# Kernel tuning notes

Measured on AMD Instinct MI355X. Metric: run time of the kernel, lower is better.

## Reference

```python
import jax, jax.numpy as jnp
import numpy as np

NEG_SLOPE = 0.01  # F.leaky_relu default


def _unfold3(x):
    # x: [B,C,H,W] -> [B,C,9,H,W] of 3x3 neighborhoods (zero pad 1)
    B, C, H, W = x.shape
    xp = jnp.pad(x, ((0, 0), (0, 0), (1, 1), (1, 1)))
    return jnp.stack([xp[:, :, i:i + H, j:j + W] for i in range(3) for j in range(3)], axis=2)


def _resize_bilinear(img, oh, ow):
    # torch F.interpolate mode='bilinear', align_corners=False, antialias=False
    B, C, H, W = img.shape
    if oh == H and ow == W:
        return img
    def coords(out, inn):
        c = jnp.maximum((jnp.arange(out, dtype=jnp.float32) + 0.5) * (inn / out) - 0.5, 0.0)
        i0 = jnp.floor(c).astype(jnp.int32)
        i1 = jnp.minimum(i0 + 1, inn - 1)
        w = c - i0.astype(jnp.float32)
        return i0, i1, w
    i0, i1, wh = coords(oh, H)
    row = img[:, :, i0, :] * (1.0 - wh)[None, None, :, None] + img[:, :, i1, :] * wh[None, None, :, None]
    j0, j1, ww = coords(ow, W)
    return row[:, :, :, j0] * (1.0 - ww) + row[:, :, :, j1] * ww


def _up2_nearest(x):
    # F.interpolate scale_factor=2 (default mode='nearest')
    return jnp.repeat(jnp.repeat(x, 2, axis=2), 2, axis=3)


def _leaky(x):
    return jnp.where(x >= 0, x, NEG_SLOPE * x)


def _pac_conv(x, guide, w):
    # PacConv2d (gaussian kernel, k=3, stride=1, pad=1, bias=False)
    g_unf = _unfold3(guide)                      # [B,Cg,9,H,W]
    diff = g_unf - guide[:, :, None]             # f_j - f_i
    kern = jnp.exp(-0.5 * jnp.sum(diff * diff, axis=1))  # [B,9,H,W]
    x_unf = _unfold3(x)                          # [B,Ci,9,H,W]
    wk = w.reshape(w.shape[0], w.shape[1], 9)    # [Co,Ci,9]
    return jnp.einsum('oik,bikhw,bkhw->bohw', wk, x_unf, kern)


def setup_inputs() -> dict:
    key = jax.random.key(0)
    ks = jax.random.split(key, 8)
    B, Cx, Hx, Wx = 4, 384, 32, 32
    Hg = Wg = 512
    x = jax.random.normal(ks[0], (B, Cx, Hx, Wx), dtype=jnp.float32)
    guide = jax.random.uniform(ks[1], (B, 3, Hg, Wg), dtype=jnp.float32)
    lin_w = jax.random.normal(ks[2], (16, 384, 1, 1), dtype=jnp.float32) * 0.05
    lin_b = jax.random.normal(ks[3], (16,), dtype=jnp.float32) * 0.05
    chans = [16, 4, 4, 4, 1]
    w0 = jax.random.normal(ks[4], (chans[1], chans[0], 3, 3), dtype=jnp.float32) * 0.1
    w1 = jax.random.normal(ks[5], (chans[2], chans[1], 3, 3), dtype=jnp.float32) * 0.1
    w2 = jax.random.normal(ks[6], (chans[3], chans[2], 3, 3), dtype=jnp.float32) * 0.1
    w3 = jax.random.normal(ks[7], (chans[4], chans[3], 3, 3), dtype=jnp.float32) * 0.1
    return {"x": x, "guide": guide, "lin_w": lin_w, "lin_b": lin_b,
            "w0": w0, "w1": w1, "w2": w2, "w3": w3}


def reference(x, guide, lin_w, lin_b, w0, w1, w2, w3):
    # crop guide to multiple of 16 (module uses shape[-1] for both dims)
    s = (guide.shape[-1] // 16) * 16
    guide = guide[..., :s, :s]
    # 1x1 conv + leaky relu
    x = jnp.einsum('oi,bihw->bohw', lin_w[:, :, 0, 0], x) + lin_b[None, :, None, None]
    x = _leaky(x)
    ws = [w0, w1, w2, w3]
    n = len(ws)
    Hg, Wg = guide.shape[2], guide.shape[3]
    for i in range(n):
        f = 2 ** (n - 1 - i)
        g = _resize_bilinear(guide, Hg // f, Wg // f)
        x = _up2_nearest(x)
        x = _pac_conv(x, g, ws[i])
        if i < n - 1:
            x = _leaky(x)
    return jax.nn.sigmoid(x)
```

## Files before the change

### kernel.cpp

```cpp
#include <hip/hip_runtime.h>
#include <math.h>

#define NEG_SLOPE 0.01f

__device__ inline float bilin(const float* __restrict__ gp, float scale, int r, int c) {
    float ch = fmaxf((r + 0.5f) * scale - 0.5f, 0.f);
    float cw = fmaxf((c + 0.5f) * scale - 0.5f, 0.f);
    int h0 = (int)ch, w0 = (int)cw;
    int h1 = min(h0 + 1, 511), w1 = min(w0 + 1, 511);
    float fh = ch - (float)h0, fw = cw - (float)w0;
    float v00 = gp[h0 * 512 + w0], v01 = gp[h0 * 512 + w1];
    float v10 = gp[h1 * 512 + w0], v11 = gp[h1 * 512 + w1];
    float top = v00 + (v01 - v00) * fw;
    float bot = v10 + (v11 - v10) * fw;
    return top + (bot - top) * fh;
}

__global__ void __launch_bounds__(256)
prep_kernel(const float* __restrict__ x, const float* __restrict__ lw,
            const float* __restrict__ lb, float* __restrict__ x16,
            const float* __restrict__ g, float* __restrict__ g64p,
            float* __restrict__ g128p, float* __restrict__ g256p) {
    int bid = blockIdx.x;
    if (bid < 256) {
        int idx = bid * 256 + threadIdx.x;
        int hw = idx & 1023, co = (idx >> 10) & 15, bb = idx >> 14;
        const float* xp = x + bb * 384 * 1024 + hw;
        const float* wp = lw + co * 384;
        float a0 = 0.f, a1 = 0.f, a2 = 0.f, a3 = 0.f;
        for (int ci = 0; ci < 384; ci += 4) {
            a0 = fmaf(wp[ci],     xp[(ci)     * 1024], a0);
            a1 = fmaf(wp[ci + 1], xp[(ci + 1) * 1024], a1);
            a2 = fmaf(wp[ci + 2], xp[(ci + 2) * 1024], a2);
            a3 = fmaf(wp[ci + 3], xp[(ci + 3) * 1024], a3);
        }
        float acc = lb[co] + ((a0 + a1) + (a2 + a3));
        x16[idx] = acc >= 0.f ? acc : NEG_SLOPE * acc;
    } else {
        int idx = (bid - 256) * 256 + threadIdx.x;
        int R; float scale; float* outp; int o;
        if (idx < 786432)      { R = 256; scale = 2.f; outp = g256p; o = idx; }
        else if (idx < 983040) { R = 128; scale = 4.f; outp = g128p; o = idx - 786432; }
        else                   { R = 64;  scale = 8.f; outp = g64p;  o = idx - 983040; }
        int c = o % R;
        int r = (o / R) % R;
        int bc = o / (R * R);
        outp[o] = bilin(g + (size_t)bc * 262144, scale, r, c);
    }
}

template <int Ci, int Co>
__device__ inline void pac_lds(const float* __restrict__ sx, int BXr, int BXc, int NX,
                               const float* __restrict__ sg, int BGr, int BGc, int NG,
                               const float* __restrict__ sw, float* __restrict__ so,
                               int BOr, int BOc, int NO, int RES) {
    const int NG2 = NG * NG, NX2 = NX * NX, NO2 = NO * NO;
    for (int i = threadIdx.x; i < NO2; i += 256) {
        int r = i / NO, c = i % NO;
        int gh = BOr + r, gw = BOc + c;
        float acc[Co];
#pragma unroll
        for (int co = 0; co < Co; ++co) acc[co] = 0.f;
        if (gh >= 0 && gh < RES && gw >= 0 && gw < RES) {
            int lc0 = (gh - BGr) * NG + (gw - BGc);
            float gc0 = sg[lc0], gc1 = sg[NG2 + lc0], gc2 = sg[2 * NG2 + lc0];
#pragma unroll
            for (int tt = 0; tt < 9; ++tt) {
                int hh = gh + tt / 3 - 1, ww = gw + tt % 3 - 1;
                if (hh < 0 || hh >= RES || ww < 0 || ww >= RES) continue;
                int lt = (hh - BGr) * NG + (ww - BGc);
                float d0 = sg[lt] - gc0;
                float d1 = sg[NG2 + lt] - gc1;
                float d2 = sg[2 * NG2 + lt] - gc2;
                float k = __expf(-0.5f * (d0 * d0 + d1 * d1 + d2 * d2));
                int lx = ((hh >> 1) - BXr) * NX + ((ww >> 1) - BXc);
#pragma unroll
                for (int ci = 0; ci < Ci; ++ci) {
                    float xv = sx[ci * NX2 + lx] * k;
#pragma unroll
                    for (int co = 0; co < Co; ++co)
                        acc[co] = fmaf(sw[(co * Ci + ci) * 9 + tt], xv, acc[co]);
                }
            }
        }
#pragma unroll
        for (int co = 0; co < Co; ++co) {
            float v = acc[co];
            so[co * NO2 + i] = v >= 0.f ? v : NEG_SLOPE * v;
        }
    }
}

__global__ void __launch_bounds__(256)
pac_mid_kernel(const float* __restrict__ x16g, const float* __restrict__ g64p,
               const float* __restrict__ g128p,
               const float* __restrict__ w0, const float* __restrict__ w1,
               float* __restrict__ x1g) {
    __shared__ float smem[3100];
    float* sw0   = smem;
    float* sw1   = smem + 576;
    float* sx16  = smem + 720;
    float* sg64  = smem + 1296;
    float* sg128 = smem + 1728;
    float* sx0   = smem + 2700;

    int bid = blockIdx.x;
    int b = bid >> 6;
    int t = (bid >> 3) & 7;
    int u = bid & 7;

    const int BXr = 4 * t - 1,  BXc = 4 * u - 1;
    const int BG0r = 8 * t - 2, BG0c = 8 * u - 2;
    const int B0r = 8 * t - 1,  B0c = 8 * u - 1;
    const int BG1r = 16 * t - 1, BG1c = 16 * u - 1;

    for (int i = threadIdx.x; i < 576; i += 256) sw0[i] = w0[i];
    for (int i = threadIdx.x; i < 144; i += 256) sw1[i] = w1[i];
    for (int i = threadIdx.x; i < 576; i += 256) {
        int ci = i / 36, rem = i % 36, r = rem / 6, c = rem % 6;
        int gr = BXr + r, gc = BXc + c;
        float v = 0.f;
        if (gr >= 0 && gr < 32 && gc >= 0 && gc < 32)
            v = x16g[((b * 16 + ci) << 10) + (gr << 5) + gc];
        sx16[i] = v;
    }
    for (int i = threadIdx.x; i < 432; i += 256) {
        int ch = i / 144, rem = i % 144, r = rem / 12, c = rem % 12;
        int gr = BG0r + r, gc = BG0c + c;
        float v = 0.f;
        if (gr >= 0 && gr < 64 && gc >= 0 && gc < 64)
            v = g64p[(b * 3 + ch) * 4096 + (gr << 6) + gc];
        sg64[i] = v;
    }
    for (int i = threadIdx.x; i < 972; i += 256) {
        int ch = i / 324, rem = i % 324, r = rem / 18, c = rem % 18;
        int gr = BG1r + r, gc = BG1c + c;
        float v = 0.f;
        if (gr >= 0 && gr < 128 && gc >= 0 && gc < 128)
            v = g128p[(b * 3 + ch) * 16384 + (gr << 7) + gc];
        sg128[i] = v;
    }
    __syncthreads();

    pac_lds<16, 4>(sx16, BXr, BXc, 6, sg64, BG0r, BG0c, 12, sw0, sx0, B0r, B0c, 10, 64);
    __syncthreads();

    {
        int i = threadIdx.x;
        int r = i >> 4, c = i & 15;
        int gh = 16 * t + r, gw = 16 * u + c;
        int lc0 = (gh - BG1r) * 18 + (gw - BG1c);
        float gc0 = sg128[lc0], gc1 = sg128[324 + lc0], gc2 = sg128[648 + lc0];
        float acc[4] = {0.f, 0.f, 0.f, 0.f};
#pragma unroll
        for (int tt = 0; tt < 9; ++tt) {
            int hh = gh + tt / 3 - 1, ww = gw + tt % 3 - 1;
            if (hh < 0 || hh >= 128 || ww < 0 || ww >= 128) continue;
            int lt = (hh - BG1r) * 18 + (ww - BG1c);
            float d0 = sg128[lt] - gc0;
            float d1 = sg128[324 + lt] - gc1;
            float d2 = sg128[648 + lt] - gc2;
            float k = __expf(-0.5f * (d0 * d0 + d1 * d1 + d2 * d2));
            int lx = ((hh >> 1) - B0r) * 10 + ((ww >> 1) - B0c);
#pragma unroll
            for (int ci = 0; ci < 4; ++ci) {
                float xv = sx0[ci * 100 + lx] * k;
#pragma unroll
                for (int co = 0; co < 4; ++co)
                    acc[co] = fmaf(sw1[(co * 4 + ci) * 9 + tt], xv, acc[co]);
            }
        }
#pragma unroll
        for (int co = 0; co < 4; ++co) {
            float v = acc[co];
            v = v >= 0.f ? v : NEG_SLOPE * v;
            x1g[((b * 4 + co) << 14) + (gh << 7) + gw] = v;
        }
    }
}

template <int Ci, int Co, int R, int ACT>
__global__ void __launch_bounds__(256)
pac_stage(const float* __restrict__ x, const float* __restrict__ g,
          const float* __restrict__ wk, float* __restrict__ out) {
    __shared__ float sw[Co * Ci * 9];
    for (int i = threadIdx.x; i < Co * Ci * 9; i += 256) sw[i] = wk[i];
    __syncthreads();

    constexpr int HW = R * R;
    constexpr int Rh = R / 2;
    constexpr int HWh = Rh * Rh;
    int idx = blockIdx.x * 256 + threadIdx.x;
    int w = idx & (R - 1);
    int h = (idx / R) & (R - 1);
    int b = idx / HW;

    const float* gb = g + (size_t)b * 3 * HW;
    int ctr = h * R + w;
    float gc0 = gb[ctr];
    float gc1 = gb[HW + ctr];
    float gc2 = gb[2 * HW + ctr];

    float acc[Co];
#pragma unroll
    for (int co = 0; co < Co; ++co) acc[co] = 0.f;

    const float* xb = x + (size_t)b * Ci * HWh;

#pragma unroll
    for (int t = 0; t < 9; ++t) {
        int dh = t / 3 - 1, dw = t % 3 - 1;
        int hh = h + dh, ww = w + dw;
        if (hh < 0 || hh >= R || ww < 0 || ww >= R) continue;
        int tap = hh * R + ww;
        float d0 = gb[tap] - gc0;
        float d1 = gb[HW + tap] - gc1;
        float d2 = gb[2 * HW + tap] - gc2;
        float k = __expf(-0.5f * (d0 * d0 + d1 * d1 + d2 * d2));
        const float* xp = xb + (hh >> 1) * Rh + (ww >> 1);
#pragma unroll
        for (int ci = 0; ci < Ci; ++ci) {
            float xv = xp[ci * HWh] * k;
#pragma unroll
            for (int co = 0; co < Co; ++co)
                acc[co] = fmaf(sw[(co * Ci + ci) * 9 + t], xv, acc[co]);
        }
    }

#pragma unroll
    for (int co = 0; co < Co; ++co) {
        float v = acc[co];
        if (ACT == 0) v = v >= 0.f ? v : NEG_SLOPE * v;
        else          v = 1.0f / (1.0f + __expf(-v));
        out[(size_t)(b * Co + co) * HW + ctr] = v;
    }
}

__global__ void __launch_bounds__(256)
pac512_quad_kernel(const float* __restrict__ x2g, const float* __restrict__ guide,
                   const float* __restrict__ w3, float* __restrict__ out) {
    __shared__ float sw[36];
    if (threadIdx.x < 36) sw[threadIdx.x] = w3[threadIdx.x];
    __syncthreads();

    int idx = blockIdx.x * 256 + threadIdx.x;
    int qw = idx & 255;
    int qh = (idx >> 8) & 255;
    int b = idx >> 16;
    int h0 = qh << 1, w0 = qw << 1;

    const float* gb = guide + (size_t)b * 3 * 262144;
    const float* xb = x2g + (size_t)b * 4 * 65536;

    float gw[3][4][4];
#pragma unroll
    for (int rr = 0; rr < 4; ++rr) {
        int gr = h0 - 1 + rr;
        bool rok = (gr >= 0 && gr < 512);
#pragma unroll
        for (int cc = 0; cc < 4; ++cc) {
            int gc = w0 - 1 + cc;
            bool ok = rok && (gc >= 0 && gc < 512);
            int a = (gr << 9) + gc;
#pragma unroll
            for (int ch = 0; ch < 3; ++ch)
                gw[ch][rr][cc] = ok ? gb[ch * 262144 + a] : 0.f;
        }
    }
    float xw[4][3][3];
#pragma unroll
    for (int rr = 0; rr < 3; ++rr) {
        int xr = qh - 1 + rr;
        bool rok = (xr >= 0 && xr < 256);
#pragma unroll
        for (int cc = 0; cc < 3; ++cc) {
            int xc = qw - 1 + cc;
            bool ok = rok && (xc >= 0 && xc < 256);
            int a = (xr << 8) + xc;
#pragma unroll
            for (int ci = 0; ci < 4; ++ci)
                xw[ci][rr][cc] = ok ? xb[ci * 65536 + a] : 0.f;
        }
    }

    float* ob = out + (size_t)b * 262144;
#pragma unroll
    for (int dr = 0; dr < 2; ++dr) {
#pragma unroll
        for (int dc = 0; dc < 2; ++dc) {
            float gc0 = gw[0][dr + 1][dc + 1];
            float gc1 = gw[1][dr + 1][dc + 1];
            float gc2 = gw[2][dr + 1][dc + 1];
            float acc = 0.f;
#pragma unroll
            for (int tt = 0; tt < 9; ++tt) {
                const int th = tt / 3, tc = tt % 3;
                int hh = h0 + dr + th - 1, ww = w0 + dc + tc - 1;
                if (hh < 0 || hh >= 512 || ww < 0 || ww >= 512) continue;
                float d0 = gw[0][dr + th][dc + tc] - gc0;
                float d1 = gw[1][dr + th][dc + tc] - gc1;
                float d2 = gw[2][dr + th][dc + tc] - gc2;
                float k = __expf(-0.5f * (d0 * d0 + d1 * d1 + d2 * d2));
                const int xr = ((dr + th - 1) >> 1) + 1;
                const int xc = ((dc + tc - 1) >> 1) + 1;
#pragma unroll
                for (int ci = 0; ci < 4; ++ci)
                    acc = fmaf(sw[ci * 9 + tt], xw[ci][xr][xc] * k, acc);
            }
            ob[((h0 + dr) << 9) + (w0 + dc)] = 1.0f / (1.0f + __expf(-acc));
        }
    }
}

extern "C" void kernel_launch(void* const* d_in, const int* in_sizes, int n_in,
                              void* d_out, int out_size, void* d_ws, size_t ws_size,
                              hipStream_t stream) {
    const float* x     = (const float*)d_in[0];
    const float* guide = (const float*)d_in[1];
    const float* lin_w = (const float*)d_in[2];
    const float* lin_b = (const float*)d_in[3];
    const float* w0    = (const float*)d_in[4];
    const float* w1    = (const float*)d_in[5];
    const float* w2    = (const float*)d_in[6];
    const float* w3    = (const float*)d_in[7];
    float* out = (float*)d_out;

    float* ws    = (float*)d_ws;
    float* x16   = ws;
    float* g64p  = x16 + 65536;
    float* g128p = g64p + 49152;
    float* g256p = g128p + 196608;
    float* x1    = g256p + 786432;
    float* x2    = x1 + 262144;

    prep_kernel<<<4288, 256, 0, stream>>>(x, lin_w, lin_b, x16, guide, g64p, g128p, g256p);
    pac_mid_kernel<<<256, 256, 0, stream>>>(x16, g64p, g128p, w0, w1, x1);
    pac_stage<4, 4, 256, 0><<<1024, 256, 0, stream>>>(x1, g256p, w2, x2);
    pac512_quad_kernel<<<1024, 256, 0, stream>>>(x2, guide, w3, out);
}
```

Measured before the change: 120.0 us.

## Fuse last two PAC stages into one LDS-tiled kernel and simplify bilinear downsampling

Replaces the separate 256-resolution PAC stage and the 512-resolution quad kernel with one kernel per 16x16 output tile. It stages the guide, the downsampled guide and the x1 halo in LDS, computes the x2 tile with overlap, then the final output, so the x2 intermediate never goes through global memory and one launch is removed. It also replaces the general bilinear resize with exact 2-tap averages, since downscaling by an integer factor with align_corners=False lands on midpoints, and makes the pac_lds tile sizes compile-time template parameters. The cost is redundant halo recomputation of x2 and more LDS use per block.

```diff
diff --git a/kernel.cpp b/kernel.cpp
--- a/kernel.cpp
+++ b/kernel.cpp
@@ -2,19 +2,6 @@
 #include <math.h>
 
 #define NEG_SLOPE 0.01f
-
-__device__ inline float bilin(const float* __restrict__ gp, float scale, int r, int c) {
-    float ch = fmaxf((r + 0.5f) * scale - 0.5f, 0.f);
-    float cw = fmaxf((c + 0.5f) * scale - 0.5f, 0.f);
-    int h0 = (int)ch, w0 = (int)cw;
-    int h1 = min(h0 + 1, 511), w1 = min(w0 + 1, 511);
-    float fh = ch - (float)h0, fw = cw - (float)w0;
-    float v00 = gp[h0 * 512 + w0], v01 = gp[h0 * 512 + w1];
-    float v10 = gp[h1 * 512 + w0], v11 = gp[h1 * 512 + w1];
-    float top = v00 + (v01 - v00) * fw;
-    float bot = v10 + (v11 - v10) * fw;
-    return top + (bot - top) * fh;
-}
 
 __global__ void __launch_bounds__(256)
 prep_kernel(const float* __restrict__ x, const float* __restrict__ lw,
@@ -38,23 +25,37 @@
         x16[idx] = acc >= 0.f ? acc : NEG_SLOPE * acc;
     } else {
         int idx = (bid - 256) * 256 + threadIdx.x;
-        int R; float scale; float* outp; int o;
-        if (idx < 786432)      { R = 256; scale = 2.f; outp = g256p; o = idx; }
-        else if (idx < 983040) { R = 128; scale = 4.f; outp = g128p; o = idx - 786432; }
-        else                   { R = 64;  scale = 8.f; outp = g64p;  o = idx - 983040; }
-        int c = o % R;
-        int r = (o / R) % R;
-        int bc = o / (R * R);
-        outp[o] = bilin(g + (size_t)bc * 262144, scale, r, c);
-    }
-}
-
-template <int Ci, int Co>
-__device__ inline void pac_lds(const float* __restrict__ sx, int BXr, int BXc, int NX,
-                               const float* __restrict__ sg, int BGr, int BGc, int NG,
+        if (idx < 786432) {
+            int o = idx;
+            int c = o & 255, r = (o >> 8) & 255, bc = o >> 16;
+            const float2* gp2 = (const float2*)(g + (size_t)bc * 262144);
+            float2 a = gp2[(2 * r) * 256 + c];
+            float2 b = gp2[(2 * r + 1) * 256 + c];
+            g256p[o] = 0.25f * ((a.x + a.y) + (b.x + b.y));
+        } else if (idx < 983040) {
+            int o = idx - 786432;
+            int c = o & 127, r = (o >> 7) & 127, bc = o >> 14;
+            const float* gp = g + (size_t)bc * 262144;
+            int a0 = (4 * r + 1) * 512 + 4 * c + 1;
+            int a1 = a0 + 512;
+            g128p[o] = 0.25f * ((gp[a0] + gp[a0 + 1]) + (gp[a1] + gp[a1 + 1]));
+        } else {
+            int o = idx - 983040;
+            int c = o & 63, r = (o >> 6) & 63, bc = o >> 12;
+            const float* gp = g + (size_t)bc * 262144;
+            int a0 = (8 * r + 3) * 512 + 8 * c + 3;
+            int a1 = a0 + 512;
+            g64p[o] = 0.25f * ((gp[a0] + gp[a0 + 1]) + (gp[a1] + gp[a1 + 1]));
+        }
+    }
+}
+
+template <int Ci, int Co, int NX, int NG, int NO, int RES>
+__device__ inline void pac_lds(const float* __restrict__ sx, int BXr, int BXc,
+                               const float* __restrict__ sg, int BGr, int BGc,
                                const float* __restrict__ sw, float* __restrict__ so,
-                               int BOr, int BOc, int NO, int RES) {
-    const int NG2 = NG * NG, NX2 = NX * NX, NO2 = NO * NO;
+                               int BOr, int BOc) {
+    constexpr int NG2 = NG * NG, NX2 = NX * NX, NO2 = NO * NO;
     for (int i = threadIdx.x; i < NO2; i += 256) {
         int r = i / NO, c = i % NO;
         int gh = BOr + r, gw = BOc + c;
@@ -142,7 +143,7 @@
     }
     __syncthreads();
 
-    pac_lds<16, 4>(sx16, BXr, BXc, 6, sg64, BG0r, BG0c, 12, sw0, sx0, B0r, B0c, 10, 64);
+    pac_lds<16, 4, 6, 12, 10, 64>(sx16, BXr, BXc, sg64, BG0r, BG0c, sw0, sx0, B0r, B0c);
     __syncthreads();
 
     {
@@ -179,136 +180,84 @@
     }
 }
 
-template <int Ci, int Co, int R, int ACT>
 __global__ void __launch_bounds__(256)
-pac_stage(const float* __restrict__ x, const float* __restrict__ g,
-          const float* __restrict__ wk, float* __restrict__ out) {
-    __shared__ float sw[Co * Ci * 9];
-    for (int i = threadIdx.x; i < Co * Ci * 9; i += 256) sw[i] = wk[i];
-    __syncthreads();
-
-    constexpr int HW = R * R;
-    constexpr int Rh = R / 2;
-    constexpr int HWh = Rh * Rh;
-    int idx = blockIdx.x * 256 + threadIdx.x;
-    int w = idx & (R - 1);
-    int h = (idx / R) & (R - 1);
-    int b = idx / HW;
-
-    const float* gb = g + (size_t)b * 3 * HW;
-    int ctr = h * R + w;
-    float gc0 = gb[ctr];
-    float gc1 = gb[HW + ctr];
-    float gc2 = gb[2 * HW + ctr];
-
-    float acc[Co];
-#pragma unroll
-    for (int co = 0; co < Co; ++co) acc[co] = 0.f;
-
-    const float* xb = x + (size_t)b * Ci * HWh;
-
-#pragma unroll
-    for (int t = 0; t < 9; ++t) {
-        int dh = t / 3 - 1, dw = t % 3 - 1;
-        int hh = h + dh, ww = w + dw;
-        if (hh < 0 || hh >= R || ww < 0 || ww >= R) continue;
-        int tap = hh * R + ww;
-        float d0 = gb[tap] - gc0;
-        float d1 = gb[HW + tap] - gc1;
-        float d2 = gb[2 * HW + tap] - gc2;
-        float k = __expf(-0.5f * (d0 * d0 + d1 * d1 + d2 * d2));
-        const float* xp = xb + (hh >> 1) * Rh + (ww >> 1);
-#pragma unroll
-        for (int ci = 0; ci < Ci; ++ci) {
-            float xv = xp[ci * HWh] * k;
-#pragma unroll
-            for (int co = 0; co < Co; ++co)
-                acc[co] = fmaf(sw[(co * Ci + ci) * 9 + t], xv, acc[co]);
-        }
-    }
-
-#pragma unroll
-    for (int co = 0; co < Co; ++co) {
-        float v = acc[co];
-        if (ACT == 0) v = v >= 0.f ? v : NEG_SLOPE * v;
-        else          v = 1.0f / (1.0f + __expf(-v));
-        out[(size_t)(b * Co + co) * HW + ctr] = v;
-    }
-}
-
-__global__ void __launch_bounds__(256)
-pac512_quad_kernel(const float* __restrict__ x2g, const float* __restrict__ guide,
-                   const float* __restrict__ w3, float* __restrict__ out) {
-    __shared__ float sw[36];
-    if (threadIdx.x < 36) sw[threadIdx.x] = w3[threadIdx.x];
-    __syncthreads();
-
-    int idx = blockIdx.x * 256 + threadIdx.x;
-    int qw = idx & 255;
-    int qh = (idx >> 8) & 255;
-    int b = idx >> 16;
-    int h0 = qh << 1, w0 = qw << 1;
+pac_de_kernel(const float* __restrict__ x1g, const float* __restrict__ guide,
+              const float* __restrict__ g256p,
+              const float* __restrict__ w2, const float* __restrict__ w3,
+              float* __restrict__ out) {
+    __shared__ float smem[2128];
+    float* sw2   = smem;
+    float* sw3   = smem + 144;
+    float* sg512 = smem + 180;
+    float* sg256 = smem + 1152;
+    float* sx1   = smem + 1584;
+    float* sx2   = smem + 1728;
+
+    int bid = blockIdx.x;
+    int b = bid >> 10;
+    int t = (bid >> 5) & 31;
+    int u = bid & 31;
+
+    const int B1r = 4 * t - 1,   B1c = 4 * u - 1;
+    const int BG2r = 8 * t - 2,  BG2c = 8 * u - 2;
+    const int B2r = 8 * t - 1,   B2c = 8 * u - 1;
+    const int BG3r = 16 * t - 1, BG3c = 16 * u - 1;
 
     const float* gb = guide + (size_t)b * 3 * 262144;
-    const float* xb = x2g + (size_t)b * 4 * 65536;
-
-    float gw[3][4][4];
-#pragma unroll
-    for (int rr = 0; rr < 4; ++rr) {
-        int gr = h0 - 1 + rr;
-        bool rok = (gr >= 0 && gr < 512);
-#pragma unroll
-        for (int cc = 0; cc < 4; ++cc) {
-            int gc = w0 - 1 + cc;
-            bool ok = rok && (gc >= 0 && gc < 512);
-            int a = (gr << 9) + gc;
-#pragma unroll
-            for (int ch = 0; ch < 3; ++ch)
-                gw[ch][rr][cc] = ok ? gb[ch * 262144 + a] : 0.f;
-        }
-    }
-    float xw[4][3][3];
-#pragma unroll
-    for (int rr = 0; rr < 3; ++rr) {
-        int xr = qh - 1 + rr;
-        bool rok = (xr >= 0 && xr < 256);
-#pragma unroll
-        for (int cc = 0; cc < 3; ++cc) {
-            int xc = qw - 1 + cc;
-            bool ok = rok && (xc >= 0 && xc < 256);
-            int a = (xr << 8) + xc;
+
+    for (int i = threadIdx.x; i < 972; i += 256) {
+        int ch = i / 324, rem = i % 324, r = rem / 18, c = rem % 18;
+        int gr = BG3r + r, gc = BG3c + c;
+        float v = 0.f;
+        if (gr >= 0 && gr < 512 && gc >= 0 && gc < 512)
+            v = gb[ch * 262144 + (gr << 9) + gc];
+        sg512[i] = v;
+    }
+    for (int i = threadIdx.x; i < 432; i += 256) {
+        int ch = i / 144, rem = i % 144, r = rem / 12, c = rem % 12;
+        int gr = BG2r + r, gc = BG2c + c;
+        float v = 0.f;
+        if (gr >= 0 && gr < 256 && gc >= 0 && gc < 256)
+            v = g256p[(b * 3 + ch) * 65536 + (gr << 8) + gc];
+        sg256[i] = v;
+    }
+    for (int i = threadIdx.x; i < 144; i += 256) {
+        int ci = i / 36, rem = i % 36, r = rem / 6, c = rem % 6;
+        int gr = B1r + r, gc = B1c + c;
+        float v = 0.f;
+        if (gr >= 0 && gr < 128 && gc >= 0 && gc < 128)
+            v = x1g[((b * 4 + ci) << 14) + (gr << 7) + gc];
+        sx1[i] = v;
+    }
+    for (int i = threadIdx.x; i < 144; i += 256) sw2[i] = w2[i];
+    for (int i = threadIdx.x; i < 36;  i += 256) sw3[i] = w3[i];
+    __syncthreads();
+
+    pac_lds<4, 4, 6, 12, 10, 256>(sx1, B1r, B1c, sg256, BG2r, BG2c, sw2, sx2, B2r, B2c);
+    __syncthreads();
+
+    {
+        int i = threadIdx.x;
+        int r = i >> 4, c = i & 15;
+        int gh = 16 * t + r, gw = 16 * u + c;
+        int lc0 = (gh - BG3r) * 18 + (gw - BG3c);
+        float gc0 = sg512[lc0], gc1 = sg512[324 + lc0], gc2 = sg512[648 + lc0];
+        float acc = 0.f;
+#pragma unroll
+        for (int tt = 0; tt < 9; ++tt) {
+            int hh = gh + tt / 3 - 1, ww = gw + tt % 3 - 1;
+            if (hh < 0 || hh >= 512 || ww < 0 || ww >= 512) continue;
+            int lt = (hh - BG3r) * 18 + (ww - BG3c);
+            float d0 = sg512[lt] - gc0;
+            float d1 = sg512[324 + lt] - gc1;
+            float d2 = sg512[648 + lt] - gc2;
+            float k = __expf(-0.5f * (d0 * d0 + d1 * d1 + d2 * d2));
+            int lx = ((hh >> 1) - B2r) * 10 + ((ww >> 1) - B2c);
 #pragma unroll
             for (int ci = 0; ci < 4; ++ci)
-                xw[ci][rr][cc] = ok ? xb[ci * 65536 + a] : 0.f;
-        }
-    }
-
-    float* ob = out + (size_t)b * 262144;
-#pragma unroll
-    for (int dr = 0; dr < 2; ++dr) {
-#pragma unroll
-        for (int dc = 0; dc < 2; ++dc) {
-            float gc0 = gw[0][dr + 1][dc + 1];
-            float gc1 = gw[1][dr + 1][dc + 1];
-            float gc2 = gw[2][dr + 1][dc + 1];
-            float acc = 0.f;
-#pragma unroll
-            for (int tt = 0; tt < 9; ++tt) {
-                const int th = tt / 3, tc = tt % 3;
-                int hh = h0 + dr + th - 1, ww = w0 + dc + tc - 1;
-                if (hh < 0 || hh >= 512 || ww < 0 || ww >= 512) continue;
-                float d0 = gw[0][dr + th][dc + tc] - gc0;
-                float d1 = gw[1][dr + th][dc + tc] - gc1;
-                float d2 = gw[2][dr + th][dc + tc] - gc2;
-                float k = __expf(-0.5f * (d0 * d0 + d1 * d1 + d2 * d2));
-                const int xr = ((dr + th - 1) >> 1) + 1;
-                const int xc = ((dc + tc - 1) >> 1) + 1;
-#pragma unroll
-                for (int ci = 0; ci < 4; ++ci)
-                    acc = fmaf(sw[ci * 9 + tt], xw[ci][xr][xc] * k, acc);
-            }
-            ob[((h0 + dr) << 9) + (w0 + dc)] = 1.0f / (1.0f + __expf(-acc));
-        }
+                acc = fmaf(sw3[ci * 9 + tt], sx2[ci * 100 + lx] * k, acc);
+        }
+        out[(size_t)b * 262144 + (gh << 9) + gw] = 1.0f / (1.0f + __expf(-acc));
     }
 }
 
@@ -331,10 +280,8 @@
     float* g128p = g64p + 49152;
     float* g256p = g128p + 196608;
     float* x1    = g256p + 786432;
-    float* x2    = x1 + 262144;
 
     prep_kernel<<<4288, 256, 0, stream>>>(x, lin_w, lin_b, x16, guide, g64p, g128p, g256p);
     pac_mid_kernel<<<256, 256, 0, stream>>>(x16, g64p, g128p, w0, w1, x1);
-    pac_stage<4, 4, 256, 0><<<1024, 256, 0, stream>>>(x1, g256p, w2, x2);
-    pac512_quad_kernel<<<1024, 256, 0, stream>>>(x2, guide, w3, out);
-}
+    pac_de_kernel<<<4096, 256, 0, stream>>>(x1, guide, g256p, w2, w3, out);
+}
```

Result: slower. 123.5 us (+2.9%).
